# Performance work log

Hardware: AMD Instinct MI355X
Metric: run time of the kernel (lower is better)

## Reference

```python
import jax, jax.numpy as jnp
import numpy as np

B_, S_, DIM, DCONV, NST, DTR = 2, 1000, 1000, 3, 16, 32


def setup_inputs() -> dict:
    key = jax.random.key(0)
    ks = jax.random.split(key, 8)
    x = jax.random.normal(ks[0], (B_, S_, DIM), dtype=jnp.float32)
    proj_w = jax.random.normal(ks[1], (DIM, DIM), dtype=jnp.float32) * 0.02
    proj_b = jax.random.normal(ks[2], (DIM,), dtype=jnp.float32) * 0.02
    conv_w = jax.random.normal(ks[3], (DIM, S_, DCONV), dtype=jnp.float32) * 0.02  # (out_ch, in_ch, k)
    deltaBC_w = jax.random.normal(ks[4], (DTR + 2 * NST, DIM), dtype=jnp.float32) * 0.02
    dt_proj_w = jax.random.normal(ks[5], (DIM, DTR), dtype=jnp.float32) * 0.02
    dt_proj_b = jax.random.normal(ks[6], (DIM,), dtype=jnp.float32) * 0.02
    A_log = jnp.log(jnp.tile(jnp.arange(1, NST + 1, dtype=jnp.float32), (DIM, 1)))  # (DIM, NST)
    Dp = jnp.ones((DIM,), dtype=jnp.float32)
    return {"x": x, "proj_w": proj_w, "proj_b": proj_b, "conv_w": conv_w,
            "deltaBC_w": deltaBC_w, "dt_proj_w": dt_proj_w, "dt_proj_b": dt_proj_b,
            "A_log": A_log, "Dp": Dp}


def _selective_scan(x, delta, A, Bm, Cm, Dp):
    # x, delta: (b,l,d); A: (d,n); Bm, Cm: (b,l,n); Dp: (d,)
    deltaA = jnp.exp(delta[..., None] * A)                     # (b,l,d,n)
    BX = (delta[..., None] * Bm[:, :, None, :]) * x[..., None]  # (b,l,d,n)

    def step(h, inp):
        dA, bx = inp
        h = dA * h + bx
        return h, h

    h0 = jnp.zeros_like(deltaA[:, 0])                          # (b,d,n)
    _, hs = jax.lax.scan(step, h0,
                         (jnp.swapaxes(deltaA, 0, 1), jnp.swapaxes(BX, 0, 1)))
    hs = jnp.swapaxes(hs, 0, 1)                                # (b,l,d,n)
    y = jnp.einsum('bldn,bln->bld', hs, Cm)
    return y + Dp * x


def _ssm(x, deltaBC_w, dt_proj_w, dt_proj_b, A_log, Dp):
    A = -jnp.exp(A_log)
    dBC = x @ deltaBC_w.T                                      # (b,l,DTR+2*NST)
    delta = dBC[..., :DTR]
    Bm = dBC[..., DTR:DTR + NST]
    Cm = dBC[..., DTR + NST:]
    delta = jax.nn.softplus(delta @ dt_proj_w.T + dt_proj_b)   # (b,l,d)
    return _selective_scan(x, delta, A, Bm, Cm, Dp)


def reference(x, proj_w, proj_b, conv_w, deltaBC_w, dt_proj_w, dt_proj_b, A_log, Dp):
    path1 = x @ proj_w.T + proj_b                              # (b,1000,dim)
    # Conv1d over the feature axis: seq dim acts as channels (as in source)
    path2 = jax.lax.conv_general_dilated(path1, conv_w, window_strides=(1,),
                                         padding=[(1, 1)],
                                         dimension_numbers=('NCH', 'OIH', 'NCH'))
    path2 = jax.nn.silu(path2)                                 # (b,dim,dim)
    path2 = _ssm(path2, deltaBC_w, dt_proj_w, dt_proj_b, A_log, Dp)
    mult = jax.nn.silu(path1) * path2                          # (b,1000,dim)
    return mult @ proj_w.T + proj_b
```

## Files before the change

### kernel.cpp

```cpp
#include <hip/hip_runtime.h>
#include <hip/hip_bf16.h>
#include <math.h>

#define B_ 2
#define S_ 1000
#define D_ 1000

constexpr int CH = 25;
constexpr int NC = 40;

typedef __attribute__((ext_vector_type(8))) short bf16x8;
typedef __attribute__((ext_vector_type(4))) float f32x4;
typedef __attribute__((ext_vector_type(4))) unsigned int u32x4;

__device__ __forceinline__ float silu_f(float v) { return v / (1.f + __expf(-v)); }

__device__ __forceinline__ void gld16(const void* g, void* l) {
  __builtin_amdgcn_global_load_lds(
      (const __attribute__((address_space(1))) unsigned int*)g,
      (__attribute__((address_space(3))) unsigned int*)l, 16, 0, 0);
}

__global__ __launch_bounds__(256) void prep(const float* __restrict__ x,
                                            const float* __restrict__ pw,
                                            const float* __restrict__ cw,
                                            const float* __restrict__ dbw,
                                            __hip_bfloat16* __restrict__ xbf,
                                            __hip_bfloat16* __restrict__ wbf,
                                            __hip_bfloat16* __restrict__ cwb,
                                            __hip_bfloat16* __restrict__ dbcwb,
                                            u32x4* __restrict__ mbf16,
                                            u32x4* __restrict__ p1t16,
                                            u32x4* __restrict__ x2b16) {
  const int bid = blockIdx.x, tid = threadIdx.x;
  if (bid < 8192) {
    int idx = bid * 256 + tid;
    int r = idx >> 10, c = idx & 1023;
    float v = 0.f;
    if (r < B_ * S_ && c < D_) v = x[(size_t)r * D_ + c];
    xbf[idx] = __float2bfloat16(v);
  } else if (bid < 12288) {
    int idx = (bid - 8192) * 256 + tid;
    int r = idx >> 10, c = idx & 1023;
    float v = 0.f;
    if (r < D_ && c < D_) v = pw[(size_t)r * D_ + c];
    wbf[idx] = __float2bfloat16(v);
  } else if (bid < 16384) {
    int idx = (bid - 12288) * 256 + tid;
    int o = idx >> 10, i = idx & 1023;
    float v0 = 0.f, v1 = 0.f, v2 = 0.f;
    if (o < D_ && i < S_) {
      const float* p = cw + ((size_t)o * S_ + i) * 3;
      v0 = p[0]; v1 = p[1]; v2 = p[2];
    }
    cwb[idx]           = __float2bfloat16(v0);
    cwb[idx + 1048576] = __float2bfloat16(v1);
    cwb[idx + 2097152] = __float2bfloat16(v2);
  } else if (bid < 17408) {
    mbf16[(bid - 16384) * 256 + tid] = u32x4{0, 0, 0, 0};
  } else if (bid < 18464) {
    p1t16[(bid - 17408) * 256 + tid] = u32x4{0, 0, 0, 0};
  } else if (bid < 19488) {
    x2b16[(bid - 18464) * 256 + tid] = u32x4{0, 0, 0, 0};
  } else {
    int idx = (bid - 19488) * 256 + tid;
    int r = idx >> 10, c = idx & 1023;
    float v = (c < D_) ? dbw[(size_t)r * D_ + c] : 0.f;
    dbcwb[idx] = __float2bfloat16(v);
  }
}

__global__ __launch_bounds__(256) void gemm3(const __hip_bfloat16* __restrict__ A,
                                             const __hip_bfloat16* __restrict__ Bt,
                                             const float* __restrict__ bias,
                                             float* __restrict__ C,
                                             int M, int N, int ldc) {
  __shared__ __hip_bfloat16 Al[3][64 * 64];
  __shared__ __hip_bfloat16 Bl[3][64 * 64];
  const int tid = threadIdx.x, lane = tid & 63, w = tid >> 6;
  const int wr = w >> 1, wc = w & 1;
  const int m0 = blockIdx.x * 64, n0 = blockIdx.y * 64;
  const int srow = lane >> 3;
  const int scg  = (lane & 7) ^ srow;
  const int fr = lane & 15, fq = lane >> 4;
  const int rc0 = fr & 7;
  const __hip_bfloat16* gA = A + (size_t)(m0 + w * 16 + srow) * 1024 + scg * 8;
  const __hip_bfloat16* gB = Bt + (size_t)(n0 + w * 16 + srow) * 1024 + scg * 8;
  f32x4 acc[2][2] = {};

#define STAGE3(buf, k0)                                     \
  {                                                         \
    gld16(gA + (k0), &Al[buf][(w * 16) * 64]);              \
    gld16(gA + 8192 + (k0), &Al[buf][(w * 16 + 8) * 64]);   \
    gld16(gB + (k0), &Bl[buf][(w * 16) * 64]);              \
    gld16(gB + 8192 + (k0), &Bl[buf][(w * 16 + 8) * 64]);   \
  }

  STAGE3(0, 0);
  STAGE3(1, 64);
  for (int t = 0; t < 16; ++t) {
    const int cur = t % 3;
    if (t < 14) {
      STAGE3((t + 2) % 3, (t + 2) * 64);
      asm volatile("s_waitcnt vmcnt(8)" ::: "memory");
    } else if (t == 14) {
      asm volatile("s_waitcnt vmcnt(4)" ::: "memory");
    } else {
      asm volatile("s_waitcnt vmcnt(0)" ::: "memory");
    }
    __builtin_amdgcn_s_barrier();
#pragma unroll
    for (int kk = 0; kk < 2; ++kk) {
      const int cg = (kk * 4 + fq) ^ rc0;
      bf16x8 af[2], bfv[2];
#pragma unroll
      for (int i = 0; i < 2; ++i)
        af[i] = *(const bf16x8*)&Al[cur][(wr * 32 + i * 16 + fr) * 64 + cg * 8];
#pragma unroll
      for (int j = 0; j < 2; ++j)
        bfv[j] = *(const bf16x8*)&Bl[cur][(wc * 32 + j * 16 + fr) * 64 + cg * 8];
#pragma unroll
      for (int i = 0; i < 2; ++i)
#pragma unroll
        for (int j = 0; j < 2; ++j)
          acc[i][j] = __builtin_amdgcn_mfma_f32_16x16x32_bf16(af[i], bfv[j], acc[i][j], 0, 0, 0);
    }
    asm volatile("s_waitcnt lgkmcnt(0)" ::: "memory");
    __builtin_amdgcn_s_barrier();
  }
#undef STAGE3

#pragma unroll
  for (int i = 0; i < 2; ++i) {
#pragma unroll
    for (int j = 0; j < 2; ++j) {
      const int mb = m0 + wr * 32 + i * 16 + fq * 4;
      const int n = n0 + wc * 32 + j * 16 + fr;
      if (n < N) {
        float bv = bias ? bias[n] : 0.f;
#pragma unroll
        for (int r = 0; r < 4; ++r)
          if (mb + r < M) C[(size_t)(mb + r) * ldc + n] = acc[i][j][r] + bv;
      }
    }
  }
}

__global__ __launch_bounds__(256) void gemm_p1(const __hip_bfloat16* __restrict__ A,
                                               const __hip_bfloat16* __restrict__ Bt,
                                               const float* __restrict__ bias,
                                               __hip_bfloat16* __restrict__ P1BF,
                                               __hip_bfloat16* __restrict__ P1T) {
  __shared__ __hip_bfloat16 Al[3][64 * 64];
  __shared__ __hip_bfloat16 Bl[3][64 * 64];
  const int tid = threadIdx.x, lane = tid & 63, w = tid >> 6;
  const int wr = w >> 1, wc = w & 1;
  const int m0 = blockIdx.x * 64, n0 = blockIdx.y * 64;
  const int srow = lane >> 3;
  const int scg  = (lane & 7) ^ srow;
  const int fr = lane & 15, fq = lane >> 4;
  const int rc0 = fr & 7;
  const __hip_bfloat16* gA = A + (size_t)(m0 + w * 16 + srow) * 1024 + scg * 8;
  const __hip_bfloat16* gB = Bt + (size_t)(n0 + w * 16 + srow) * 1024 + scg * 8;
  f32x4 acc[2][2] = {};

#define STAGEP(buf, k0)                                     \
  {                                                         \
    gld16(gA + (k0), &Al[buf][(w * 16) * 64]);              \
    gld16(gA + 8192 + (k0), &Al[buf][(w * 16 + 8) * 64]);   \
    gld16(gB + (k0), &Bl[buf][(w * 16) * 64]);              \
    gld16(gB + 8192 + (k0), &Bl[buf][(w * 16 + 8) * 64]);   \
  }

  STAGEP(0, 0);
  STAGEP(1, 64);
  for (int t = 0; t < 16; ++t) {
    const int cur = t % 3;
    if (t < 14) {
      STAGEP((t + 2) % 3, (t + 2) * 64);
      asm volatile("s_waitcnt vmcnt(8)" ::: "memory");
    } else if (t == 14) {
      asm volatile("s_waitcnt vmcnt(4)" ::: "memory");
    } else {
      asm volatile("s_waitcnt vmcnt(0)" ::: "memory");
    }
    __builtin_amdgcn_s_barrier();
#pragma unroll
    for (int kk = 0; kk < 2; ++kk) {
      const int cg = (kk * 4 + fq) ^ rc0;
      bf16x8 af[2], bfv[2];
#pragma unroll
      for (int i = 0; i < 2; ++i)
        af[i] = *(const bf16x8*)&Al[cur][(wr * 32 + i * 16 + fr) * 64 + cg * 8];
#pragma unroll
      for (int j = 0; j < 2; ++j)
        bfv[j] = *(const bf16x8*)&Bl[cur][(wc * 32 + j * 16 + fr) * 64 + cg * 8];
#pragma unroll
      for (int i = 0; i < 2; ++i)
#pragma unroll
        for (int j = 0; j < 2; ++j)
          acc[i][j] = __builtin_amdgcn_mfma_f32_16x16x32_bf16(af[i], bfv[j], acc[i][j], 0, 0, 0);
    }
    asm volatile("s_waitcnt lgkmcnt(0)" ::: "memory");
    __builtin_amdgcn_s_barrier();
  }
#undef STAGEP

  float pv[2][2][4];
#pragma unroll
  for (int i = 0; i < 2; ++i)
#pragma unroll
    for (int j = 0; j < 2; ++j) {
      const int n = n0 + wc * 32 + j * 16 + fr;
      const float bv = (n < D_) ? bias[n] : 0.f;
#pragma unroll
      for (int r = 0; r < 4; ++r) pv[i][j][r] = acc[i][j][r] + bv;
    }

#pragma unroll
  for (int i = 0; i < 2; ++i) {
#pragma unroll
    for (int j = 0; j < 2; ++j) {
      const int mb = m0 + wr * 32 + i * 16 + fq * 4;
      const int n = n0 + wc * 32 + j * 16 + fr;
#pragma unroll
      for (int r = 0; r < 4; ++r)
        P1BF[(size_t)(mb + r) * 1024 + n] = __float2bfloat16(pv[i][j][r]);
    }
  }

  __hip_bfloat16* st = &Al[0][0] + w * 512;
#pragma unroll
  for (int j = 0; j < 2; ++j) {
    __syncthreads();
#pragma unroll
    for (int i = 0; i < 2; ++i)
#pragma unroll
      for (int r = 0; r < 4; ++r)
        st[fr * 32 + i * 16 + fq * 4 + r] = __float2bfloat16(pv[i][j][r]);
    __syncthreads();
    const int n_row = n0 + wc * 32 + j * 16 + (lane >> 2);
    const int mg = m0 + wr * 32 + (lane & 3) * 8;
    if (n_row < D_ && mg < B_ * S_) {
      const int bb = (mg >= S_) ? 1 : 0;
      const int s0 = mg - bb * S_;
      bf16x8 v = *(const bf16x8*)&st[(lane >> 2) * 32 + (lane & 3) * 8];
      *(bf16x8*)&P1T[((size_t)bb * 1056 + n_row + 1) * 1024 + s0] = v;
    }
  }
}

__global__ __launch_bounds__(256) void conv3(const __hip_bfloat16* __restrict__ Wt,
                                             const __hip_bfloat16* __restrict__ P1T,
                                             float* __restrict__ X2,
                                             __hip_bfloat16* __restrict__ X2B) {
  __shared__ __hip_bfloat16 Al[2][3 * 64 * 64];
  __shared__ __hip_bfloat16 Bl[2][72 * 64];
  const int b = blockIdx.z;
  const int m0 = blockIdx.x * 64, n0 = blockIdx.y * 64;
  const int tid = threadIdx.x, lane = tid & 63, w = tid >> 6;
  const int wr = w >> 1, wc = w & 1;
  const int srow = lane >> 3;
  const int scg  = (lane & 7) ^ srow;
  const int fr = lane & 15, fq = lane >> 4;
  const int rc0 = fr & 7;
  const __hip_bfloat16* gA = Wt + (size_t)(m0 + w * 16 + srow) * 1024 + scg * 8;
  const __hip_bfloat16* gB = P1T + ((size_t)b * 1056 + n0 + w * 16 + srow) * 1024 + scg * 8;
  const __hip_bfloat16* gB2 = P1T + ((size_t)b * 1056 + n0 + 64 + srow) * 1024 + scg * 8;
  f32x4 acc[2][2] = {};

#define CSTAGE(buf, k0)                                                          \
  {                                                                              \
    _Pragma("unroll")                                                            \
    for (int q = 0; q < 3; ++q) {                                                \
      gld16(gA + (size_t)q * 1048576 + (k0), &Al[buf][q * 4096 + (w * 16) * 64]);\
      gld16(gA + (size_t)q * 1048576 + 8192 + (k0),                              \
            &Al[buf][q * 4096 + (w * 16 + 8) * 64]);                             \
    }                                                                            \
    gld16(gB + (k0), &Bl[buf][(w * 16) * 64]);                                   \
    gld16(gB + 8192 + (k0), &Bl[buf][(w * 16 + 8) * 64]);                        \
    if (w == 0) gld16(gB2 + (k0), &Bl[buf][64 * 64]);                            \
  }

  CSTAGE(0, 0);
  for (int t = 0; t < 16; ++t) {
    const int cur = t & 1;
    if (t < 15) {
      CSTAGE(cur ^ 1, (t + 1) * 64);
      if (w == 0) asm volatile("s_waitcnt vmcnt(9)" ::: "memory");
      else        asm volatile("s_waitcnt vmcnt(8)" ::: "memory");
    } else {
      asm volatile("s_waitcnt vmcnt(0)" ::: "memory");
    }
    __builtin_amdgcn_s_barrier();
#pragma unroll
    for (int q = 0; q < 3; ++q) {
      const int rcq = (fr + q) & 7;
#pragma unroll
      for (int kk = 0; kk < 2; ++kk) {
        const int cga = (kk * 4 + fq) ^ rc0;
        const int cgb = (kk * 4 + fq) ^ rcq;
        bf16x8 af[2], bfv[2];
#pragma unroll
        for (int i = 0; i < 2; ++i)
          af[i] = *(const bf16x8*)&Al[cur][q * 4096 + (wr * 32 + i * 16 + fr) * 64 + cga * 8];
#pragma unroll
        for (int j = 0; j < 2; ++j)
          bfv[j] = *(const bf16x8*)&Bl[cur][(wc * 32 + j * 16 + fr + q) * 64 + cgb * 8];
#pragma unroll
        for (int i = 0; i < 2; ++i)
#pragma unroll
          for (int j = 0; j < 2; ++j)
            acc[i][j] = __builtin_amdgcn_mfma_f32_16x16x32_bf16(af[i], bfv[j], acc[i][j], 0, 0, 0);
      }
    }
    asm volatile("s_waitcnt lgkmcnt(0)" ::: "memory");
    __builtin_amdgcn_s_barrier();
  }
#undef CSTAGE

#pragma unroll
  for (int i = 0; i < 2; ++i) {
#pragma unroll
    for (int j = 0; j < 2; ++j) {
      const int ob = m0 + wr * 32 + i * 16 + fq * 4;
      const int h = n0 + wc * 32 + j * 16 + fr;
      if (h < D_) {
#pragma unroll
        for (int r = 0; r < 4; ++r)
          if (ob + r < S_) {
            float v = silu_f(acc[i][j][r]);
            X2[((size_t)b * S_ + ob + r) * D_ + h] = v;
            X2B[(size_t)(b * S_ + ob + r) * 1024 + h] = __float2bfloat16(v);
          }
      }
    }
  }
}

__global__ __launch_bounds__(256) void gemm_dbc(const __hip_bfloat16* __restrict__ A,
                                                const __hip_bfloat16* __restrict__ Bt,
                                                float* __restrict__ part) {
  __shared__ __hip_bfloat16 Al[3][64 * 64];
  __shared__ __hip_bfloat16 Bl[3][64 * 64];
  const int tid = threadIdx.x, lane = tid & 63, w = tid >> 6;
  const int wr = w >> 1, wc = w & 1;
  const int m0 = blockIdx.x * 64;
  const int kb = blockIdx.y * 256;
  const int srow = lane >> 3;
  const int scg  = (lane & 7) ^ srow;
  const int fr = lane & 15, fq = lane >> 4;
  const int rc0 = fr & 7;
  const __hip_bfloat16* gA = A + (size_t)(m0 + w * 16 + srow) * 1024 + scg * 8 + kb;
  const __hip_bfloat16* gB = Bt + (size_t)(w * 16 + srow) * 1024 + scg * 8 + kb;
  f32x4 acc[2][2] = {};

#define STAGED(buf, k0)                                     \
  {                                                         \
    gld16(gA + (k0), &Al[buf][(w * 16) * 64]);              \
    gld16(gA + 8192 + (k0), &Al[buf][(w * 16 + 8) * 64]);   \
    gld16(gB + (k0), &Bl[buf][(w * 16) * 64]);              \
    gld16(gB + 8192 + (k0), &Bl[buf][(w * 16 + 8) * 64]);   \
  }

  STAGED(0, 0);
  STAGED(1, 64);
  for (int t = 0; t < 4; ++t) {
    const int cur = t % 3;
    if (t < 2) {
      STAGED((t + 2) % 3, (t + 2) * 64);
      asm volatile("s_waitcnt vmcnt(8)" ::: "memory");
    } else if (t == 2) {
      asm volatile("s_waitcnt vmcnt(4)" ::: "memory");
    } else {
      asm volatile("s_waitcnt vmcnt(0)" ::: "memory");
    }
    __builtin_amdgcn_s_barrier();
#pragma unroll
    for (int kk = 0; kk < 2; ++kk) {
      const int cg = (kk * 4 + fq) ^ rc0;
      bf16x8 af[2], bfv[2];
#pragma unroll
      for (int i = 0; i < 2; ++i)
        af[i] = *(const bf16x8*)&Al[cur][(wr * 32 + i * 16 + fr) * 64 + cg * 8];
#pragma unroll
      for (int j = 0; j < 2; ++j)
        bfv[j] = *(const bf16x8*)&Bl[cur][(wc * 32 + j * 16 + fr) * 64 + cg * 8];
#pragma unroll
      for (int i = 0; i < 2; ++i)
#pragma unroll
        for (int j = 0; j < 2; ++j)
          acc[i][j] = __builtin_amdgcn_mfma_f32_16x16x32_bf16(af[i], bfv[j], acc[i][j], 0, 0, 0);
    }
    asm volatile("s_waitcnt lgkmcnt(0)" ::: "memory");
    __builtin_amdgcn_s_barrier();
  }
#undef STAGED

  float* pb = part + (size_t)blockIdx.y * 2048 * 64;
#pragma unroll
  for (int i = 0; i < 2; ++i) {
#pragma unroll
    for (int j = 0; j < 2; ++j) {
      const int mb = m0 + wr * 32 + i * 16 + fq * 4;
      const int n = wc * 32 + j * 16 + fr;
#pragma unroll
      for (int r = 0; r < 4; ++r)
        pb[(size_t)(mb + r) * 64 + n] = acc[i][j][r];
    }
  }
}

__global__ __launch_bounds__(256) void delta_red(const float* __restrict__ part,
                                                 const float* __restrict__ W,
                                                 const float* __restrict__ bias,
                                                 float* __restrict__ delta,
                                                 float* __restrict__ dbc) {
  const int mBase = blockIdx.y * 16;
  if (blockIdx.x == 4) {
    for (int e = threadIdx.x; e < 512; e += 256) {
      int r = e >> 5, c = (e & 31) + 32;
      size_t off = (size_t)(mBase + r) * 64 + c;
      float s = 0.f;
#pragma unroll
      for (int kc = 0; kc < 4; ++kc) s += part[(size_t)kc * 2048 * 64 + off];
      dbc[off] = s;
    }
    return;
  }
  const int d = blockIdx.x * 256 + threadIdx.x;
  __shared__ float rs[16][32];
  for (int idx = threadIdx.x; idx < 512; idx += 256) {
    int r = idx >> 5, c = idx & 31;
    size_t off = (size_t)(mBase + r) * 64 + c;
    float s = 0.f;
#pragma unroll
    for (int kc = 0; kc < 4; ++kc) s += part[(size_t)kc * 2048 * 64 + off];
    rs[r][c] = s;
  }
  __syncthreads();
  if (d >= D_) return;
  float w[32];
#pragma unroll
  for (int j = 0; j < 32; ++j) w[j] = W[d * 32 + j];
  const float bb = bias[d];
  for (int r = 0; r < 16; ++r) {
    float acc = bb;
#pragma unroll
    for (int j = 0; j < 32; ++j) acc = fmaf(rs[r][j], w[j], acc);
    float sp = (acc > 20.f) ? acc : log1pf(__expf(acc));
    delta[(size_t)(mBase + r) * D_ + d] = sp;
  }
}

__global__ __launch_bounds__(256) void scan1(const float* __restrict__ delta,
                                             const float* __restrict__ x2,
                                             const float* __restrict__ dBC,
                                             float* __restrict__ hfin,
                                             float* __restrict__ psum) {
  const int d = blockIdx.x * 256 + threadIdx.x;
  const int c = blockIdx.y, b = blockIdx.z;
  __shared__ float Bs[CH][16];
  for (int idx = threadIdx.x; idx < CH * 16; idx += 256) {
    int r = idx >> 4, n = idx & 15;
    Bs[r][n] = dBC[(size_t)(b * S_ + c * CH + r) * 64 + 32 + n];
  }
  __syncthreads();
  if (d >= D_) return;
  float h[16] = {};
  float dsum = 0.f;
  const float* dp = delta + ((size_t)(b * S_ + c * CH)) * D_ + d;
  const float* xp = x2 + ((size_t)(b * S_ + c * CH)) * D_ + d;
  for (int l = 0; l < CH; ++l) {
    float dlt = dp[(size_t)l * D_];
    float xv = xp[(size_t)l * D_];
    dsum += dlt;
    float dx = dlt * xv;
    float E = __expf(-dlt);
    float da = 1.f;
#pragma unroll
    for (int n = 0; n < 16; ++n) {
      da *= E;
      h[n] = fmaf(da, h[n], dx * Bs[l][n]);
    }
  }
  float* hb = hfin + (((size_t)b * NC + c) * D_ + d) * 16;
#pragma unroll
  for (int n = 0; n < 16; ++n) hb[n] = h[n];
  psum[((size_t)b * NC + c) * D_ + d] = dsum;
}

__global__ __launch_bounds__(256) void scan2(const float* __restrict__ hfin,
                                             const float* __restrict__ psum,
                                             float* __restrict__ hin) {
  const int t = blockIdx.x * 256 + threadIdx.x;
  if (t >= B_ * D_ * 16) return;
  const int n = t & 15;
  const int bd = t >> 4;
  const int b = bd / D_, d = bd - b * D_;
  const float a = -(float)(n + 1);
  float h = 0.f;
  for (int c = 0; c < NC; ++c) {
    const size_t base = ((size_t)b * NC + c) * D_ + d;
    hin[base * 16 + n] = h;
    float ps = psum[base];
    float hf = hfin[base * 16 + n];
    h = fmaf(__expf(a * ps), h, hf);
  }
}

__global__ __launch_bounds__(256) void scan3(const float* __restrict__ delta,
                                             const float* __restrict__ x2,
                                             const float* __restrict__ dBC,
                                             const float* __restrict__ Dp,
                                             const float* __restrict__ hin,
                                             const __hip_bfloat16* __restrict__ p1b,
                                             __hip_bfloat16* __restrict__ mbf) {
  const int d = blockIdx.x * 256 + threadIdx.x;
  const int c = blockIdx.y, b = blockIdx.z;
  __shared__ float Bs[CH][16];
  __shared__ float Cs[CH][16];
  for (int idx = threadIdx.x; idx < CH * 32; idx += 256) {
    int r = idx >> 5, col = idx & 31;
    float v = dBC[(size_t)(b * S_ + c * CH + r) * 64 + 32 + col];
    if (col < 16) Bs[r][col] = v;
    else Cs[r][col - 16] = v;
  }
  __syncthreads();
  if (d >= D_) return;
  float h[16];
  const float* hp = hin + (((size_t)b * NC + c) * D_ + d) * 16;
#pragma unroll
  for (int n = 0; n < 16; ++n) h[n] = hp[n];
  const float dpv = Dp[d];
  const float* dp = delta + ((size_t)(b * S_ + c * CH)) * D_ + d;
  const float* xp = x2 + ((size_t)(b * S_ + c * CH)) * D_ + d;
  const __hip_bfloat16* pp = p1b + ((size_t)(b * S_ + c * CH)) * 1024 + d;
  __hip_bfloat16* mp = mbf + ((size_t)(b * S_ + c * CH)) * 1024 + d;
  for (int l = 0; l < CH; ++l) {
    float dlt = dp[(size_t)l * D_];
    float xv = xp[(size_t)l * D_];
    float dx = dlt * xv;
    float E = __expf(-dlt);
    float da = 1.f;
    float yv = 0.f;
#pragma unroll
    for (int n = 0; n < 16; ++n) {
      da *= E;
      h[n] = fmaf(da, h[n], dx * Bs[l][n]);
      yv = fmaf(h[n], Cs[l][n], yv);
    }
    float y = fmaf(dpv, xv, yv);
    float pv = __bfloat162float(pp[(size_t)l * 1024]);
    mp[(size_t)l * 1024] = __float2bfloat16(silu_f(pv) * y);
  }
}

extern "C" void kernel_launch(void* const* d_in, const int* in_sizes, int n_in,
                              void* d_out, int out_size, void* d_ws, size_t ws_size,
                              hipStream_t stream) {
  const float* x        = (const float*)d_in[0];
  const float* proj_w   = (const float*)d_in[1];
  const float* proj_b   = (const float*)d_in[2];
  const float* conv_w   = (const float*)d_in[3];
  const float* deltaBC_w= (const float*)d_in[4];
  const float* dt_proj_w= (const float*)d_in[5];
  const float* dt_proj_b= (const float*)d_in[6];
  const float* Dp       = (const float*)d_in[8];
  float* out = (float*)d_out;

  char* w8 = (char*)d_ws;
  float* X2    = (float*)(w8 + 0);
  float* DBC   = (float*)(w8 + 8000000);
  float* DELTA = (float*)(w8 + 8512000);
  float* HFIN  = (float*)(w8 + 16512000);
  float* PSUM  = (float*)(w8 + 21632000);
  float* HIN   = (float*)(w8 + 21952000);
  __hip_bfloat16* XBF   = (__hip_bfloat16*)(w8 + 27072000);
  __hip_bfloat16* WBF   = (__hip_bfloat16*)(w8 + 31266304);
  __hip_bfloat16* CWB   = (__hip_bfloat16*)(w8 + 33363456);
  __hip_bfloat16* P1T   = (__hip_bfloat16*)(w8 + 39654912);
  __hip_bfloat16* MBF   = (__hip_bfloat16*)(w8 + 43980288);
  __hip_bfloat16* P1BF  = (__hip_bfloat16*)(w8 + 48174592);
  __hip_bfloat16* X2B   = (__hip_bfloat16*)(w8 + 52368896);
  __hip_bfloat16* DBCWB = (__hip_bfloat16*)(w8 + 56563200);
  float* PART  = (float*)(w8 + 56694272);

  dim3 blk(256);
  prep<<<dim3(19744), blk, 0, stream>>>(x, proj_w, conv_w, deltaBC_w,
                                        XBF, WBF, CWB, DBCWB,
                                        (u32x4*)MBF, (u32x4*)P1T, (u32x4*)X2B);
  gemm_p1<<<dim3(32, 16), blk, 0, stream>>>(XBF, WBF, proj_b, P1BF, P1T);
  conv3<<<dim3(16, 16, B_), blk, 0, stream>>>(CWB, P1T, X2, X2B);
  gemm_dbc<<<dim3(32, 4), blk, 0, stream>>>(X2B, DBCWB, PART);
  delta_red<<<dim3(5, 125), blk, 0, stream>>>(PART, dt_proj_w, dt_proj_b, DELTA, DBC);
  scan1<<<dim3(4, NC, B_), blk, 0, stream>>>(DELTA, X2, DBC, HFIN, PSUM);
  scan2<<<dim3(125), blk, 0, stream>>>(HFIN, PSUM, HIN);
  scan3<<<dim3(4, NC, B_), blk, 0, stream>>>(DELTA, X2, DBC, Dp, HIN, P1BF, MBF);
  gemm3<<<dim3(32, 16), blk, 0, stream>>>(MBF, WBF, proj_b, out, B_ * S_, D_, D_);
}
```

Before: 118.6 us.

## Drop fp32 conv output, widen conv tile, zero only padding regions

The conv kernel now writes only the bf16 X2B buffer, and the scan kernels read that instead of the fp32 X2 copy. This removes an 8 MB fp32 store plus the fp32 reads in both scan passes. The conv kernel moves to 512 threads with a 64x128 output tile, so the shared P1T rows are reused across more columns. The prep kernel now zeroes only the padding columns and rows of MBF, X2B and P1T instead of the whole buffers. In exchange, the scan uses bf16-rounded conv activations, which loses some precision.

```diff
diff --git a/kernel.cpp b/kernel.cpp
--- a/kernel.cpp
+++ b/kernel.cpp
@@ -11,7 +11,6 @@
 
 typedef __attribute__((ext_vector_type(8))) short bf16x8;
 typedef __attribute__((ext_vector_type(4))) float f32x4;
-typedef __attribute__((ext_vector_type(4))) unsigned int u32x4;
 
 __device__ __forceinline__ float silu_f(float v) { return v / (1.f + __expf(-v)); }
 
@@ -29,10 +28,11 @@
                                             __hip_bfloat16* __restrict__ wbf,
                                             __hip_bfloat16* __restrict__ cwb,
                                             __hip_bfloat16* __restrict__ dbcwb,
-                                            u32x4* __restrict__ mbf16,
-                                            u32x4* __restrict__ p1t16,
-                                            u32x4* __restrict__ x2b16) {
+                                            __hip_bfloat16* __restrict__ mbf,
+                                            __hip_bfloat16* __restrict__ p1t,
+                                            __hip_bfloat16* __restrict__ x2b) {
   const int bid = blockIdx.x, tid = threadIdx.x;
+  const __hip_bfloat16 z = __float2bfloat16(0.f);
   if (bid < 8192) {
     int idx = bid * 256 + tid;
     int r = idx >> 10, c = idx & 1023;
@@ -56,17 +56,33 @@
     cwb[idx]           = __float2bfloat16(v0);
     cwb[idx + 1048576] = __float2bfloat16(v1);
     cwb[idx + 2097152] = __float2bfloat16(v2);
-  } else if (bid < 17408) {
-    mbf16[(bid - 16384) * 256 + tid] = u32x4{0, 0, 0, 0};
-  } else if (bid < 18464) {
-    p1t16[(bid - 17408) * 256 + tid] = u32x4{0, 0, 0, 0};
-  } else if (bid < 19488) {
-    x2b16[(bid - 18464) * 256 + tid] = u32x4{0, 0, 0, 0};
-  } else {
-    int idx = (bid - 19488) * 256 + tid;
+  } else if (bid < 16640) {
+    int idx = (bid - 16384) * 256 + tid;
     int r = idx >> 10, c = idx & 1023;
     float v = (c < D_) ? dbw[(size_t)r * D_ + c] : 0.f;
     dbcwb[idx] = __float2bfloat16(v);
+  } else {
+    int idx = (bid - 16640) * 256 + tid;
+    if (idx < 49152) {
+      mbf[(size_t)(idx / 24) * 1024 + 1000 + idx % 24] = z;
+    } else if (idx < 98304) {
+      int i2 = idx - 49152;
+      x2b[(size_t)(i2 / 24) * 1024 + 1000 + i2 % 24] = z;
+    } else if (idx < 212992) {
+      int j = idx - 98304;
+      int bb = j / 57344;
+      int rr = (j % 57344) >> 10;
+      int col = j & 1023;
+      int row = (rr == 0) ? 0 : 1000 + rr;
+      p1t[((size_t)bb * 1056 + row) * 1024 + col] = z;
+    } else if (idx < 260992) {
+      int k = idx - 212992;
+      int bb = k / 24000;
+      int rem = k % 24000;
+      int row = 1 + rem / 24;
+      int col = 1000 + rem % 24;
+      p1t[((size_t)bb * 1056 + row) * 1024 + col] = z;
+    }
   }
 }
 
@@ -250,45 +266,51 @@
   }
 }
 
-__global__ __launch_bounds__(256) void conv3(const __hip_bfloat16* __restrict__ Wt,
+__global__ __launch_bounds__(512) void conv5(const __hip_bfloat16* __restrict__ Wt,
                                              const __hip_bfloat16* __restrict__ P1T,
-                                             float* __restrict__ X2,
                                              __hip_bfloat16* __restrict__ X2B) {
   __shared__ __hip_bfloat16 Al[2][3 * 64 * 64];
-  __shared__ __hip_bfloat16 Bl[2][72 * 64];
+  __shared__ __hip_bfloat16 Bl[2][136 * 64];
   const int b = blockIdx.z;
-  const int m0 = blockIdx.x * 64, n0 = blockIdx.y * 64;
+  const int m0 = blockIdx.x * 64, n0 = blockIdx.y * 128;
   const int tid = threadIdx.x, lane = tid & 63, w = tid >> 6;
-  const int wr = w >> 1, wc = w & 1;
+  const int wr = w >> 2, wc = w & 3;
   const int srow = lane >> 3;
   const int scg  = (lane & 7) ^ srow;
   const int fr = lane & 15, fq = lane >> 4;
   const int rc0 = fr & 7;
-  const __hip_bfloat16* gA = Wt + (size_t)(m0 + w * 16 + srow) * 1024 + scg * 8;
-  const __hip_bfloat16* gB = P1T + ((size_t)b * 1056 + n0 + w * 16 + srow) * 1024 + scg * 8;
-  const __hip_bfloat16* gB2 = P1T + ((size_t)b * 1056 + n0 + 64 + srow) * 1024 + scg * 8;
+  const __hip_bfloat16* gW = Wt + (size_t)(m0 + srow) * 1024 + scg * 8;
+  const __hip_bfloat16* gP = P1T + ((size_t)b * 1056 + n0 + srow) * 1024 + scg * 8;
   f32x4 acc[2][2] = {};
 
-#define CSTAGE(buf, k0)                                                          \
-  {                                                                              \
-    _Pragma("unroll")                                                            \
-    for (int q = 0; q < 3; ++q) {                                                \
-      gld16(gA + (size_t)q * 1048576 + (k0), &Al[buf][q * 4096 + (w * 16) * 64]);\
-      gld16(gA + (size_t)q * 1048576 + 8192 + (k0),                              \
-            &Al[buf][q * 4096 + (w * 16 + 8) * 64]);                             \
-    }                                                                            \
-    gld16(gB + (k0), &Bl[buf][(w * 16) * 64]);                                   \
-    gld16(gB + 8192 + (k0), &Bl[buf][(w * 16 + 8) * 64]);                        \
-    if (w == 0) gld16(gB2 + (k0), &Bl[buf][64 * 64]);                            \
-  }
-
-  CSTAGE(0, 0);
+#define C5STG(buf, k0)                                                     \
+  {                                                                        \
+    _Pragma("unroll")                                                      \
+    for (int tt = 0; tt < 3; ++tt) {                                       \
+      int aj = w * 3 + tt, q = aj >> 3, rg = aj & 7;                       \
+      gld16(gW + (size_t)q * 1048576 + rg * 8192 + (k0),                   \
+            &Al[buf][q * 4096 + rg * 512]);                                \
+    }                                                                      \
+    if (w == 0) {                                                          \
+      _Pragma("unroll")                                                    \
+      for (int bj = 0; bj < 3; ++bj)                                       \
+        gld16(gP + bj * 8192 + (k0), &Bl[buf][bj * 512]);                  \
+    } else {                                                               \
+      _Pragma("unroll")                                                    \
+      for (int u = 0; u < 2; ++u) {                                        \
+        int bj = 2 * w + 1 + u;                                            \
+        gld16(gP + bj * 8192 + (k0), &Bl[buf][bj * 512]);                  \
+      }                                                                    \
+    }                                                                      \
+  }
+
+  C5STG(0, 0);
   for (int t = 0; t < 16; ++t) {
     const int cur = t & 1;
     if (t < 15) {
-      CSTAGE(cur ^ 1, (t + 1) * 64);
-      if (w == 0) asm volatile("s_waitcnt vmcnt(9)" ::: "memory");
-      else        asm volatile("s_waitcnt vmcnt(8)" ::: "memory");
+      C5STG(cur ^ 1, (t + 1) * 64);
+      if (w == 0) asm volatile("s_waitcnt vmcnt(6)" ::: "memory");
+      else        asm volatile("s_waitcnt vmcnt(5)" ::: "memory");
     } else {
       asm volatile("s_waitcnt vmcnt(0)" ::: "memory");
     }
@@ -317,7 +339,7 @@
     asm volatile("s_waitcnt lgkmcnt(0)" ::: "memory");
     __builtin_amdgcn_s_barrier();
   }
-#undef CSTAGE
+#undef C5STG
 
 #pragma unroll
   for (int i = 0; i < 2; ++i) {
@@ -328,11 +350,9 @@
       if (h < D_) {
 #pragma unroll
         for (int r = 0; r < 4; ++r)
-          if (ob + r < S_) {
-            float v = silu_f(acc[i][j][r]);
-            X2[((size_t)b * S_ + ob + r) * D_ + h] = v;
-            X2B[(size_t)(b * S_ + ob + r) * 1024 + h] = __float2bfloat16(v);
-          }
+          if (ob + r < S_)
+            X2B[(size_t)(b * S_ + ob + r) * 1024 + h] =
+                __float2bfloat16(silu_f(acc[i][j][r]));
       }
     }
   }
@@ -454,7 +474,7 @@
 }
 
 __global__ __launch_bounds__(256) void scan1(const float* __restrict__ delta,
-                                             const float* __restrict__ x2,
+                                             const __hip_bfloat16* __restrict__ x2b,
                                              const float* __restrict__ dBC,
                                              float* __restrict__ hfin,
                                              float* __restrict__ psum) {
@@ -470,10 +490,10 @@
   float h[16] = {};
   float dsum = 0.f;
   const float* dp = delta + ((size_t)(b * S_ + c * CH)) * D_ + d;
-  const float* xp = x2 + ((size_t)(b * S_ + c * CH)) * D_ + d;
+  const __hip_bfloat16* xp = x2b + ((size_t)(b * S_ + c * CH)) * 1024 + d;
   for (int l = 0; l < CH; ++l) {
     float dlt = dp[(size_t)l * D_];
-    float xv = xp[(size_t)l * D_];
+    float xv = __bfloat162float(xp[(size_t)l * 1024]);
     dsum += dlt;
     float dx = dlt * xv;
     float E = __expf(-dlt);
@@ -510,7 +530,7 @@
 }
 
 __global__ __launch_bounds__(256) void scan3(const float* __restrict__ delta,
-                                             const float* __restrict__ x2,
+                                             const __hip_bfloat16* __restrict__ x2b,
                                              const float* __restrict__ dBC,
                                              const float* __restrict__ Dp,
                                              const float* __restrict__ hin,
@@ -534,12 +554,12 @@
   for (int n = 0; n < 16; ++n) h[n] = hp[n];
   const float dpv = Dp[d];
   const float* dp = delta + ((size_t)(b * S_ + c * CH)) * D_ + d;
-  const float* xp = x2 + ((size_t)(b * S_ + c * CH)) * D_ + d;
+  const __hip_bfloat16* xp = x2b + ((size_t)(b * S_ + c * CH)) * 1024 + d;
   const __hip_bfloat16* pp = p1b + ((size_t)(b * S_ + c * CH)) * 1024 + d;
   __hip_bfloat16* mp = mbf + ((size_t)(b * S_ + c * CH)) * 1024 + d;
   for (int l = 0; l < CH; ++l) {
     float dlt = dp[(size_t)l * D_];
-    float xv = xp[(size_t)l * D_];
+    float xv = __bfloat162float(xp[(size_t)l * 1024]);
     float dx = dlt * xv;
     float E = __expf(-dlt);
     float da = 1.f;
@@ -570,32 +590,30 @@
   float* out = (float*)d_out;
 
   char* w8 = (char*)d_ws;
-  float* X2    = (float*)(w8 + 0);
-  float* DBC   = (float*)(w8 + 8000000);
-  float* DELTA = (float*)(w8 + 8512000);
-  float* HFIN  = (float*)(w8 + 16512000);
-  float* PSUM  = (float*)(w8 + 21632000);
-  float* HIN   = (float*)(w8 + 21952000);
-  __hip_bfloat16* XBF   = (__hip_bfloat16*)(w8 + 27072000);
-  __hip_bfloat16* WBF   = (__hip_bfloat16*)(w8 + 31266304);
-  __hip_bfloat16* CWB   = (__hip_bfloat16*)(w8 + 33363456);
-  __hip_bfloat16* P1T   = (__hip_bfloat16*)(w8 + 39654912);
-  __hip_bfloat16* MBF   = (__hip_bfloat16*)(w8 + 43980288);
-  __hip_bfloat16* P1BF  = (__hip_bfloat16*)(w8 + 48174592);
-  __hip_bfloat16* X2B   = (__hip_bfloat16*)(w8 + 52368896);
-  __hip_bfloat16* DBCWB = (__hip_bfloat16*)(w8 + 56563200);
-  float* PART  = (float*)(w8 + 56694272);
+  float* DBC   = (float*)(w8 + 0);
+  float* DELTA = (float*)(w8 + 512000);
+  float* HFIN  = (float*)(w8 + 8512000);
+  float* PSUM  = (float*)(w8 + 13632000);
+  float* HIN   = (float*)(w8 + 13952000);
+  __hip_bfloat16* XBF   = (__hip_bfloat16*)(w8 + 19072000);
+  __hip_bfloat16* WBF   = (__hip_bfloat16*)(w8 + 23266304);
+  __hip_bfloat16* CWB   = (__hip_bfloat16*)(w8 + 25363456);
+  __hip_bfloat16* P1T   = (__hip_bfloat16*)(w8 + 31654912);
+  __hip_bfloat16* MBF   = (__hip_bfloat16*)(w8 + 35980288);
+  __hip_bfloat16* P1BF  = (__hip_bfloat16*)(w8 + 40174592);
+  __hip_bfloat16* X2B   = (__hip_bfloat16*)(w8 + 44368896);
+  __hip_bfloat16* DBCWB = (__hip_bfloat16*)(w8 + 48563200);
+  float* PART  = (float*)(w8 + 48694272);
 
   dim3 blk(256);
-  prep<<<dim3(19744), blk, 0, stream>>>(x, proj_w, conv_w, deltaBC_w,
-                                        XBF, WBF, CWB, DBCWB,
-                                        (u32x4*)MBF, (u32x4*)P1T, (u32x4*)X2B);
+  prep<<<dim3(17660), blk, 0, stream>>>(x, proj_w, conv_w, deltaBC_w,
+                                        XBF, WBF, CWB, DBCWB, MBF, P1T, X2B);
   gemm_p1<<<dim3(32, 16), blk, 0, stream>>>(XBF, WBF, proj_b, P1BF, P1T);
-  conv3<<<dim3(16, 16, B_), blk, 0, stream>>>(CWB, P1T, X2, X2B);
+  conv5<<<dim3(16, 8, B_), dim3(512), 0, stream>>>(CWB, P1T, X2B);
   gemm_dbc<<<dim3(32, 4), blk, 0, stream>>>(X2B, DBCWB, PART);
   delta_red<<<dim3(5, 125), blk, 0, stream>>>(PART, dt_proj_w, dt_proj_b, DELTA, DBC);
-  scan1<<<dim3(4, NC, B_), blk, 0, stream>>>(DELTA, X2, DBC, HFIN, PSUM);
+  scan1<<<dim3(4, NC, B_), blk, 0, stream>>>(DELTA, X2B, DBC, HFIN, PSUM);
   scan2<<<dim3(125), blk, 0, stream>>>(HFIN, PSUM, HIN);
-  scan3<<<dim3(4, NC, B_), blk, 0, stream>>>(DELTA, X2, DBC, Dp, HIN, P1BF, MBF);
+  scan3<<<dim3(4, NC, B_), blk, 0, stream>>>(DELTA, X2B, DBC, Dp, HIN, P1BF, MBF);
   gemm3<<<dim3(32, 16), blk, 0, stream>>>(MBF, WBF, proj_b, out, B_ * S_, D_, D_);
 }
```

Measured after the change: 117.7 us. No clear change (-0.8%).
